# Performance work log

Hardware: AMD Instinct MI355X
Metric: run time of the kernel (lower is better)

Reference implementation:

```python
import jax, jax.numpy as jnp
import numpy as np

B, H, W, C = 8, 256, 256, 64
M1, M2 = 32, 32
SCALE = 1.0 / (C * C)


def setup_inputs() -> dict:
    key = jax.random.key(0)
    ku, k1, k2, k3, k4 = jax.random.split(key, 5)
    u = jax.random.normal(ku, (B, H, W, C), dtype=jnp.float32)
    wshape = (C, C, M1, M2)
    w_pos_r = SCALE * jax.random.normal(k1, wshape, dtype=jnp.float32)
    w_pos_i = SCALE * jax.random.normal(k2, wshape, dtype=jnp.float32)
    w_neg_r = SCALE * jax.random.normal(k3, wshape, dtype=jnp.float32)
    w_neg_i = SCALE * jax.random.normal(k4, wshape, dtype=jnp.float32)
    return {"u": u, "w_pos_r": w_pos_r, "w_pos_i": w_pos_i,
            "w_neg_r": w_neg_r, "w_neg_i": w_neg_i}


def _compl_mul2d(inp, weights):
    # inp: [B, m1, m2, Cin] complex; weights: [Cin, Cout, m1, m2] complex
    return jnp.einsum('bxyi,ioxy->bxyo', inp, weights)


def reference(u, w_pos_r, w_pos_i, w_neg_r, w_neg_i):
    b, h, w, c = u.shape
    wf = w // 2 + 1  # rfft size along W
    u_ft = jnp.fft.rfft2(u, axes=(1, 2))  # [B, H, Wf, C] complex
    w_pos = jax.lax.complex(w_pos_r, w_pos_i)
    w_neg = jax.lax.complex(w_neg_r, w_neg_i)
    top = _compl_mul2d(u_ft[:, :M1, :M2, :], w_pos)   # low positive freqs
    bot = _compl_mul2d(u_ft[:, h - M1:, :M2, :], w_neg)  # low negative freqs
    # out_ft zero-initialized, only truncated modes populated.
    # (Original allocates [B,H,W,C] but irfft2 with s=(H,W) only reads
    #  the first W//2+1 columns, which equals this [B,H,Wf,C] tensor.)
    out_ft = jnp.zeros((b, h, wf, c), dtype=u_ft.dtype)
    out_ft = out_ft.at[:, :M1, :M2, :].set(top)
    out_ft = out_ft.at[:, h - M1:, :M2, :].set(bot)
    # out_ft[:, -M1:M1] assignment in original is an empty slice (M1 <= H/2): no-op.
    return jnp.fft.irfft2(out_ft, s=(h, w), axes=(1, 2)).astype(u.dtype)
```

## Files before the change

kernel.cpp:

```cpp
#include <hip/hip_runtime.h>
#include <math.h>

#define BB 8
#define HH 256
#define WW 256
#define CC 64

__device__ inline void cmac(float2& a, float tx, float ty, float2 v) {
    a.x += tx * v.x - ty * v.y;
    a.y += tx * v.y + ty * v.x;
}
__device__ inline void fma4(float4& a, float s, float4 v) {
    a.x += s * v.x; a.y += s * v.y; a.z += s * v.z; a.w += s * v.w;
}

__global__ __launch_bounds__(256) void k_tw(float2* __restrict__ Tf,
                                            float2* __restrict__ Ti,
                                            float* __restrict__ Ty,
                                            float* __restrict__ T2) {
    int e = blockIdx.x * 256 + threadIdx.x;
    if (e < 16384) {
        int x = e >> 6;
        int j = e & 63;
        int kxa = j + ((j >> 5) * 192);
        int tt = (kxa * x) & 255;
        float ang = (float)tt * (6.283185307179586f / 256.0f);
        float s, c;
        sincosf(ang, &s, &c);
        Tf[(size_t)x * 64 + j] = make_float2(c, -s);
        const float k = 2.0f / 65536.0f;
        Ti[(size_t)j * 256 + x] = make_float2(c * k, s * k);
    } else {
        int f = e - 16384;
        if (f < 8192) {
            int yp = f >> 6;
            int col = f & 63;
            int par = (col >> 5) & 1;
            int cs = (col >> 4) & 1;
            int m = col & 15;
            int ky = 2 * m + par;
            int tt = (ky * yp) & 255;
            float ang = (float)tt * (6.283185307179586f / 256.0f);
            float s, c;
            sincosf(ang, &s, &c);
            Ty[f] = cs ? -s : c;
        } else {
            int g = f - 8192;
            int pi = g >> 12;
            int j = (g >> 7) & 31;
            int p = g & 127;
            int m = j >> 1, ri = j & 1;
            int ky = 2 * m + pi;
            int tt = (ky * p) & 255;
            float ang = (float)tt * (6.283185307179586f / 256.0f);
            float s, c;
            sincosf(ang, &s, &c);
            T2[g] = ri ? -s : c;
        }
    }
}

__global__ __launch_bounds__(128, 3) void k_fwd_y(const float* __restrict__ u,
                                                  const float* __restrict__ Ty,
                                                  float2* __restrict__ V) {
    __shared__ float ue[32 * 68];
    __shared__ float uo[32 * 68];
    __shared__ float Tt[32 * 68];

    int t = threadIdx.x;
    int b = blockIdx.x >> 8;
    int x = blockIdx.x & 255;
    int i8 = (t & 7) * 8;
    int w = t >> 3;
    int p = w & 1;
    int kyq = w >> 1;
    int yy = t >> 2;
    int c0 = (t & 3) * 16;

    const float* ub = u + ((size_t)(b * HH + x)) * (WW * CC);
    const float* uplane = p ? uo : ue;

    float4 A0r = {0,0,0,0}, A0i = {0,0,0,0};
    float4 B0r = {0,0,0,0}, B0i = {0,0,0,0};
    float4 A1r = {0,0,0,0}, A1i = {0,0,0,0};
    float4 B1r = {0,0,0,0}, B1i = {0,0,0,0};

    for (int yt = 0; yt < 4; ++yt) {
        const float* plo = ub + (size_t)(yt * 32 + yy) * CC + c0;
        const float* phi = plo + 128 * CC;
        float4 l0 = *(const float4*)(plo);
        float4 l1 = *(const float4*)(plo + 4);
        float4 l2 = *(const float4*)(plo + 8);
        float4 l3 = *(const float4*)(plo + 12);
        float4 h0 = *(const float4*)(phi);
        float4 h1 = *(const float4*)(phi + 4);
        float4 h2 = *(const float4*)(phi + 8);
        float4 h3 = *(const float4*)(phi + 12);
        const float* tsrc = Ty + (size_t)(yt * 32 + yy) * 64 + c0;
        float4 t0 = *(const float4*)(tsrc);
        float4 t1 = *(const float4*)(tsrc + 4);
        float4 t2 = *(const float4*)(tsrc + 8);
        float4 t3 = *(const float4*)(tsrc + 12);

        __syncthreads();
        int wb = yy * 68 + c0;
        *(float4*)(ue + wb)      = make_float4(l0.x+h0.x, l0.y+h0.y, l0.z+h0.z, l0.w+h0.w);
        *(float4*)(ue + wb + 4)  = make_float4(l1.x+h1.x, l1.y+h1.y, l1.z+h1.z, l1.w+h1.w);
        *(float4*)(ue + wb + 8)  = make_float4(l2.x+h2.x, l2.y+h2.y, l2.z+h2.z, l2.w+h2.w);
        *(float4*)(ue + wb + 12) = make_float4(l3.x+h3.x, l3.y+h3.y, l3.z+h3.z, l3.w+h3.w);
        *(float4*)(uo + wb)      = make_float4(l0.x-h0.x, l0.y-h0.y, l0.z-h0.z, l0.w-h0.w);
        *(float4*)(uo + wb + 4)  = make_float4(l1.x-h1.x, l1.y-h1.y, l1.z-h1.z, l1.w-h1.w);
        *(float4*)(uo + wb + 8)  = make_float4(l2.x-h2.x, l2.y-h2.y, l2.z-h2.z, l2.w-h2.w);
        *(float4*)(uo + wb + 12) = make_float4(l3.x-h3.x, l3.y-h3.y, l3.z-h3.z, l3.w-h3.w);
        *(float4*)(Tt + wb)      = t0;
        *(float4*)(Tt + wb + 4)  = t1;
        *(float4*)(Tt + wb + 8)  = t2;
        *(float4*)(Tt + wb + 12) = t3;
        __syncthreads();

        #pragma unroll
        for (int y2 = 0; y2 < 32; ++y2) {
            const float* tb = Tt + y2 * 68 + p * 32 + kyq * 2;
            float2 cp = *(const float2*)(tb);
            float2 sp = *(const float2*)(tb + 16);
            const float* up = uplane + y2 * 68 + i8;
            float4 uq0 = *(const float4*)(up);
            float4 uq1 = *(const float4*)(up + 4);
            fma4(A0r, cp.x, uq0);  fma4(A0i, sp.x, uq0);
            fma4(B0r, cp.x, uq1);  fma4(B0i, sp.x, uq1);
            fma4(A1r, cp.y, uq0);  fma4(A1i, sp.y, uq0);
            fma4(B1r, cp.y, uq1);  fma4(B1i, sp.y, uq1);
        }
    }

    {
        int ky = 4 * kyq + p;
        float2* vp = V + (size_t)(b * HH + x) * 2048 + ky * 64 + i8;
        *(float4*)(vp)     = make_float4(A0r.x, A0i.x, A0r.y, A0i.y);
        *(float4*)(vp + 2) = make_float4(A0r.z, A0i.z, A0r.w, A0i.w);
        *(float4*)(vp + 4) = make_float4(B0r.x, B0i.x, B0r.y, B0i.y);
        *(float4*)(vp + 6) = make_float4(B0r.z, B0i.z, B0r.w, B0i.w);
    }
    {
        int ky = 4 * kyq + 2 + p;
        float2* vp = V + (size_t)(b * HH + x) * 2048 + ky * 64 + i8;
        *(float4*)(vp)     = make_float4(A1r.x, A1i.x, A1r.y, A1i.y);
        *(float4*)(vp + 2) = make_float4(A1r.z, A1i.z, A1r.w, A1i.w);
        *(float4*)(vp + 4) = make_float4(B1r.x, B1i.x, B1r.y, B1i.y);
        *(float4*)(vp + 6) = make_float4(B1r.z, B1i.z, B1r.w, B1i.w);
    }
}

__global__ __launch_bounds__(256) void k_fwd_x(const float2* __restrict__ Tf,
                                               const float2* __restrict__ V,
                                               float2* __restrict__ U) {
    __shared__ float sRe[2 * 2048];
    __shared__ float sIm[2 * 2048];
    __shared__ float2 Ts[32 * 16];

    int bx = blockIdx.x;
    int jq = bx >> 8;
    int ky = bx & 31;
    int b  = (bx >> 5) & 7;
    int t = threadIdx.x;
    int jr = t >> 5;
    int ir = t & 31;

    float2 a00 = {0,0}, a01 = {0,0}, a10 = {0,0}, a11 = {0,0};

    const float2* vb = V + (size_t)b * (HH * 2048) + ky * 64;
    int vrow = t >> 3;
    int vcol = (t & 7) * 8;
    int tjj = (t & 7) * 2;
    int parOff = (jr & 1) * 2048;

    for (int x0 = 0; x0 < 128; x0 += 32) {
        const float2* plo = vb + (size_t)(x0 + vrow) * 2048 + vcol;
        const float2* phi = plo + 128 * 2048;
        float4 l0 = *(const float4*)(plo);
        float4 l1 = *(const float4*)(plo + 2);
        float4 l2 = *(const float4*)(plo + 4);
        float4 l3 = *(const float4*)(plo + 6);
        float4 h0 = *(const float4*)(phi);
        float4 h1 = *(const float4*)(phi + 2);
        float4 h2 = *(const float4*)(phi + 4);
        float4 h3 = *(const float4*)(phi + 6);
        float4 tv = *(const float4*)(Tf + (size_t)(x0 + vrow) * 64 + jq * 16 + tjj);

        __syncthreads();
        *(float4*)&Ts[vrow * 16 + tjj] = tv;
        int wb = vrow * 64 + vcol;
        *(float4*)(sRe + wb)            = make_float4(l0.x+h0.x, l0.z+h0.z, l1.x+h1.x, l1.z+h1.z);
        *(float4*)(sRe + wb + 4)        = make_float4(l2.x+h2.x, l2.z+h2.z, l3.x+h3.x, l3.z+h3.z);
        *(float4*)(sIm + wb)            = make_float4(l0.y+h0.y, l0.w+h0.w, l1.y+h1.y, l1.w+h1.w);
        *(float4*)(sIm + wb + 4)        = make_float4(l2.y+h2.y, l2.w+h2.w, l3.y+h3.y, l3.w+h3.w);
        *(float4*)(sRe + 2048 + wb)     = make_float4(l0.x-h0.x, l0.z-h0.z, l1.x-h1.x, l1.z-h1.z);
        *(float4*)(sRe + 2048 + wb + 4) = make_float4(l2.x-h2.x, l2.z-h2.z, l3.x-h3.x, l3.z-h3.z);
        *(float4*)(sIm + 2048 + wb)     = make_float4(l0.y-h0.y, l0.w-h0.w, l1.y-h1.y, l1.w-h1.w);
        *(float4*)(sIm + 2048 + wb + 4) = make_float4(l2.y-h2.y, l2.w-h2.w, l3.y-h3.y, l3.w-h3.w);
        __syncthreads();

        #pragma unroll
        for (int xx = 0; xx < 32; ++xx) {
            float2 t0 = Ts[xx * 16 + jr];
            float2 t1 = Ts[xx * 16 + jr + 8];
            const float* re = sRe + parOff + xx * 64;
            const float* im = sIm + parOff + xx * 64;
            float vr0 = re[ir], vr1 = re[ir + 32];
            float vi0 = im[ir], vi1 = im[ir + 32];
            a00.x += t0.x*vr0 - t0.y*vi0;  a00.y += t0.x*vi0 + t0.y*vr0;
            a01.x += t0.x*vr1 - t0.y*vi1;  a01.y += t0.x*vi1 + t0.y*vr1;
            a10.x += t1.x*vr0 - t1.y*vi0;  a10.y += t1.x*vi0 + t1.y*vr0;
            a11.x += t1.x*vr1 - t1.y*vi1;  a11.y += t1.x*vi1 + t1.y*vr1;
        }
    }

    int j0 = jq * 16 + jr;
    float2* u0 = U + ((size_t)(j0 * 32 + ky) * 8 + b) * 64 + ir;
    u0[0]  = a00;
    u0[32] = a01;
    float2* u1 = U + ((size_t)((j0 + 8) * 32 + ky) * 8 + b) * 64 + ir;
    u1[0]  = a10;
    u1[32] = a11;
}

__global__ __launch_bounds__(256) void k_modew(const float* __restrict__ wpr,
                                               const float* __restrict__ wpi,
                                               const float* __restrict__ wnr,
                                               const float* __restrict__ wni,
                                               const float2* __restrict__ U,
                                               float2* __restrict__ OF) {
    __shared__ float2 uS[4 * 8 * 64];
    __shared__ float2 wS[4 * 8 * 32];

    int bx = blockIdx.x;
    int j   = bx & 63;
    int kyt = (bx >> 6) & 7;
    int oh  = bx >> 9;
    int ky0 = kyt * 4;
    int sel = j >> 5, kxl = j & 31;
    const float* sr = sel ? wnr : wpr;
    const float* si = sel ? wni : wpi;
    int tid = threadIdx.x;

    const float2* up = U + (size_t)(j * 32 + ky0) * 512;
    #pragma unroll
    for (int k = 0; k < 8; ++k) uS[tid + 256 * k] = up[tid + 256 * k];

    int o32 = tid & 31;
    int bh  = tid >> 5;
    int irS = tid >> 5;
    int ooS = tid & 31;

    float2 acc[4];
    #pragma unroll
    for (int k = 0; k < 4; ++k) acc[k] = make_float2(0.f, 0.f);

    for (int it = 0; it < 8; ++it) {
        __syncthreads();
        {
            int ig = it * 8 + irS;
            int og = oh * 32 + ooS;
            size_t base = (((size_t)(ig * 64 + og)) * 32 + kxl) * 32 + ky0;
            float4 r0 = *(const float4*)(sr + base);
            float4 q0 = *(const float4*)(si + base);
            float2* wrow = wS + irS * 32 + ooS;
            wrow[0 * 256] = make_float2(r0.x, q0.x);
            wrow[1 * 256] = make_float2(r0.y, q0.y);
            wrow[2 * 256] = make_float2(r0.z, q0.z);
            wrow[3 * 256] = make_float2(r0.w, q0.w);
        }
        __syncthreads();
        #pragma unroll
        for (int ir = 0; ir < 8; ++ir) {
            int ig = it * 8 + ir;
            #pragma unroll
            for (int ky = 0; ky < 4; ++ky) {
                float2 wv = wS[ky * 256 + ir * 32 + o32];
                float2 uv = uS[ky * 512 + bh * 64 + ig];
                acc[ky].x += uv.x * wv.x - uv.y * wv.y;
                acc[ky].y += uv.x * wv.y + uv.y * wv.x;
            }
        }
    }

    int og = oh * 32 + o32;
    #pragma unroll
    for (int ky = 0; ky < 4; ++ky) {
        OF[((size_t)(bh * 32 + ky0 + ky) * 64 + j) * 64 + og] = acc[ky];
    }
}

__global__ __launch_bounds__(256) void k_inv_x(const float2* __restrict__ Ti,
                                               const float2* __restrict__ OF,
                                               float2* __restrict__ A) {
    __shared__ float2 Ts[32 * 32];
    __shared__ float2 Os[32 * 64];

    int bx = blockIdx.x;
    int xt = bx >> 8;
    int ky = bx & 31;
    int b  = (bx >> 5) & 7;
    int t = threadIdx.x;
    int or_ = t & 15;
    int xr = t >> 4;

    float2 acc[2][2][4];
    #pragma unroll
    for (int pa = 0; pa < 2; ++pa)
        #pragma unroll
        for (int p = 0; p < 2; ++p)
            #pragma unroll
            for (int q = 0; q < 4; ++q) acc[pa][p][q] = make_float2(0.f, 0.f);

    const float2* ofb = OF + (size_t)(b * 32 + ky) * 4096;
    int sj = t >> 3;
    int sx = (t & 7) * 4;
    int so = (t & 7) * 8;

    for (int kh = 0; kh < 2; ++kh) {
        const float2* tsrc = Ti + (size_t)(kh * 32 + sj) * 256 + xt * 32 + sx;
        float4 t0 = *(const float4*)(tsrc);
        float4 t1 = *(const float4*)(tsrc + 2);
        const float2* osrc = ofb + (size_t)(kh * 32 + sj) * 64 + so;
        float4 o0 = *(const float4*)(osrc);
        float4 o1 = *(const float4*)(osrc + 2);
        float4 o2 = *(const float4*)(osrc + 4);
        float4 o3 = *(const float4*)(osrc + 6);

        __syncthreads();
        *(float4*)&Ts[sj * 32 + sx]     = t0;
        *(float4*)&Ts[sj * 32 + sx + 2] = t1;
        float2* od = &Os[sj * 64 + so];
        *(float4*)(od)     = o0;
        *(float4*)(od + 2) = o1;
        *(float4*)(od + 4) = o2;
        *(float4*)(od + 6) = o3;
        __syncthreads();

        #pragma unroll
        for (int jj = 0; jj < 32; ++jj) {
            float4 tp = *(const float4*)&Ts[jj * 32 + xr * 2];
            float2 q0 = Os[jj * 64 + or_];
            float2 q1 = Os[jj * 64 + or_ + 16];
            float2 q2 = Os[jj * 64 + or_ + 32];
            float2 q3 = Os[jj * 64 + or_ + 48];
            const int pa = jj & 1;
            cmac(acc[pa][0][0], tp.x, tp.y, q0);
            cmac(acc[pa][0][1], tp.x, tp.y, q1);
            cmac(acc[pa][0][2], tp.x, tp.y, q2);
            cmac(acc[pa][0][3], tp.x, tp.y, q3);
            cmac(acc[pa][1][0], tp.z, tp.w, q0);
            cmac(acc[pa][1][1], tp.z, tp.w, q1);
            cmac(acc[pa][1][2], tp.z, tp.w, q2);
            cmac(acc[pa][1][3], tp.z, tp.w, q3);
        }
    }

    float sc = (ky == 0) ? 0.5f : 1.0f;
    #pragma unroll
    for (int p = 0; p < 2; ++p) {
        int x = xt * 32 + xr * 2 + p;
        float2* alo = A + ((size_t)(b * 256 + x) * 32 + ky) * 64 + or_;
        float2* ahi = A + ((size_t)(b * 256 + x + 128) * 32 + ky) * 64 + or_;
        #pragma unroll
        for (int q = 0; q < 4; ++q) {
            float2 se = acc[0][p][q], so2 = acc[1][p][q];
            alo[16 * q] = make_float2((se.x + so2.x) * sc, (se.y + so2.y) * sc);
            ahi[16 * q] = make_float2((se.x - so2.x) * sc, (se.y - so2.y) * sc);
        }
    }
}

__global__ __launch_bounds__(512, 2) void k_inv_y(const float* __restrict__ T2g,
                                                  const float2* __restrict__ A,
                                                  float* __restrict__ out) {
    __shared__ float As[2 * 32 * 68];
    __shared__ float T2s[2 * 32 * 132];

    int t = threadIdx.x;
    int b = blockIdx.x >> 8;
    int x = blockIdx.x & 255;
    int o4 = (t & 15) * 4;
    int pr = t >> 4;

    float acc[2][4][4];
    #pragma unroll
    for (int pi = 0; pi < 2; ++pi)
        #pragma unroll
        for (int pp = 0; pp < 4; ++pp)
            #pragma unroll
            for (int k = 0; k < 4; ++k) acc[pi][pp][k] = 0.f;

    {
        int ky = t >> 4;
        int oc = (t & 15) * 4;
        const float2* ap = A + (size_t)(b * 256 + x) * 2048 + ky * 64 + oc;
        float4 g0 = *(const float4*)(ap);
        float4 g1 = *(const float4*)(ap + 2);
        int pi = ky & 1, m = ky >> 1;
        float* re = As + ((pi * 32) + 2 * m) * 68 + oc;
        float* im = As + ((pi * 32) + 2 * m + 1) * 68 + oc;
        *(float4*)(re) = make_float4(g0.x, g0.z, g1.x, g1.z);
        *(float4*)(im) = make_float4(g0.y, g0.w, g1.y, g1.w);
    }
    {
        int row = t >> 3;
        int c = (t & 7) * 16;
        const float* tg = T2g + (size_t)row * 128 + c;
        float4 q0 = *(const float4*)(tg);
        float4 q1 = *(const float4*)(tg + 4);
        float4 q2 = *(const float4*)(tg + 8);
        float4 q3 = *(const float4*)(tg + 12);
        float* td = T2s + row * 132 + c;
        *(float4*)(td)      = q0;
        *(float4*)(td + 4)  = q1;
        *(float4*)(td + 8)  = q2;
        *(float4*)(td + 12) = q3;
    }
    __syncthreads();

    #pragma unroll
    for (int pi = 0; pi < 2; ++pi) {
        #pragma unroll
        for (int jj = 0; jj < 32; ++jj) {
            float4 ta = *(const float4*)(T2s + (pi * 32 + jj) * 132 + pr * 4);
            float4 av = *(const float4*)(As + (pi * 32 + jj) * 68 + o4);
            acc[pi][0][0] += ta.x * av.x;  acc[pi][0][1] += ta.x * av.y;
            acc[pi][0][2] += ta.x * av.z;  acc[pi][0][3] += ta.x * av.w;
            acc[pi][1][0] += ta.y * av.x;  acc[pi][1][1] += ta.y * av.y;
            acc[pi][1][2] += ta.y * av.z;  acc[pi][1][3] += ta.y * av.w;
            acc[pi][2][0] += ta.z * av.x;  acc[pi][2][1] += ta.z * av.y;
            acc[pi][2][2] += ta.z * av.z;  acc[pi][2][3] += ta.z * av.w;
            acc[pi][3][0] += ta.w * av.x;  acc[pi][3][1] += ta.w * av.y;
            acc[pi][3][2] += ta.w * av.z;  acc[pi][3][3] += ta.w * av.w;
        }
    }

    float* op = out + (size_t)(b * 256 + x) * (256 * 64);
    #pragma unroll
    for (int pp = 0; pp < 4; ++pp) {
        int p = pr * 4 + pp;
        float4 lo = make_float4(acc[0][pp][0] + acc[1][pp][0],
                                acc[0][pp][1] + acc[1][pp][1],
                                acc[0][pp][2] + acc[1][pp][2],
                                acc[0][pp][3] + acc[1][pp][3]);
        float4 hi = make_float4(acc[0][pp][0] - acc[1][pp][0],
                                acc[0][pp][1] - acc[1][pp][1],
                                acc[0][pp][2] - acc[1][pp][2],
                                acc[0][pp][3] - acc[1][pp][3]);
        *(float4*)(op + (size_t)p * 64 + o4)         = lo;
        *(float4*)(op + (size_t)(p + 128) * 64 + o4) = hi;
    }
}

extern "C" void kernel_launch(void* const* d_in, const int* in_sizes, int n_in,
                              void* d_out, int out_size, void* d_ws, size_t ws_size,
                              hipStream_t stream) {
    const float* u   = (const float*)d_in[0];
    const float* wpr = (const float*)d_in[1];
    const float* wpi = (const float*)d_in[2];
    const float* wnr = (const float*)d_in[3];
    const float* wni = (const float*)d_in[4];
    float* out = (float*)d_out;

    char* ws = (char*)d_ws;
    float2* U  = (float2*)(ws);
    float2* OF = (float2*)(ws + 8388608);
    float2* V  = (float2*)(ws + 16777216);
    float2* A  = V;
    float2* Tf = (float2*)(ws + 50331648);
    float2* Ti = (float2*)(ws + 50331648 + 131072);
    float*  Ty = (float*)(ws + 50331648 + 262144);
    float*  T2 = (float*)(ws + 50331648 + 262144 + 32768);

    k_tw<<<128, 256, 0, stream>>>(Tf, Ti, Ty, T2);
    k_fwd_y<<<BB * HH, 128, 0, stream>>>(u, Ty, V);
    k_fwd_x<<<1024, 256, 0, stream>>>(Tf, V, U);
    k_modew<<<1024, 256, 0, stream>>>(wpr, wpi, wnr, wni, U, OF);
    k_inv_x<<<1024, 256, 0, stream>>>(Ti, OF, A);
    k_inv_y<<<BB * HH, 512, 0, stream>>>(T2, A, out);
}
```

Baseline: 224.1 us.

## Retile forward-y and inverse-y DFT kernels for more register reuse per thread

k_fwd_y now processes four x rows per 256-thread block. Each thread computes four frequency pairs instead of two, using 16-row y tiles, so every twiddle tile loaded into shared memory is reused across four rows. k_inv_y drops from 512 to 128 threads per block, and each thread computes an 8x8 output tile instead of 4x4, which cuts shared-memory loads per FMA. The cost is higher register pressure and fewer threads in flight for latency hiding, with a risk of lower occupancy.

```diff
diff --git a/kernel.cpp b/kernel.cpp
--- a/kernel.cpp
+++ b/kernel.cpp
@@ -60,33 +60,41 @@
     }
 }
 
-__global__ __launch_bounds__(128, 3) void k_fwd_y(const float* __restrict__ u,
-                                                  const float* __restrict__ Ty,
-                                                  float2* __restrict__ V) {
-    __shared__ float ue[32 * 68];
-    __shared__ float uo[32 * 68];
-    __shared__ float Tt[32 * 68];
+__global__ __launch_bounds__(256) void k_fwd_y(const float* __restrict__ u,
+                                               const float* __restrict__ Ty,
+                                               float2* __restrict__ V) {
+    __shared__ float ue[4][16 * 68];
+    __shared__ float uo[4][16 * 68];
+    __shared__ float Tt[16 * 68];
 
     int t = threadIdx.x;
-    int b = blockIdx.x >> 8;
-    int x = blockIdx.x & 255;
-    int i8 = (t & 7) * 8;
-    int w = t >> 3;
+    int bx = blockIdx.x;
+    int b = bx >> 6;
+    int x4 = (bx & 63) * 4;
+    int r = t >> 6;
+    int l = t & 63;
+    int x = x4 + r;
+    int i8 = (l & 7) * 8;
+    int w = l >> 3;
     int p = w & 1;
-    int kyq = w >> 1;
-    int yy = t >> 2;
-    int c0 = (t & 3) * 16;
+    int kq = w >> 1;
+    int yy = l >> 2;
+    int c0 = (l & 3) * 16;
+    int trow = t >> 4;
+    int tc = (t & 15) * 4;
 
     const float* ub = u + ((size_t)(b * HH + x)) * (WW * CC);
-    const float* uplane = p ? uo : ue;
-
-    float4 A0r = {0,0,0,0}, A0i = {0,0,0,0};
-    float4 B0r = {0,0,0,0}, B0i = {0,0,0,0};
-    float4 A1r = {0,0,0,0}, A1i = {0,0,0,0};
-    float4 B1r = {0,0,0,0}, B1i = {0,0,0,0};
-
-    for (int yt = 0; yt < 4; ++yt) {
-        const float* plo = ub + (size_t)(yt * 32 + yy) * CC + c0;
+    const float* uplane = p ? uo[r] : ue[r];
+
+    float4 aR[4], aI[4], bR[4], bI[4];
+    #pragma unroll
+    for (int m = 0; m < 4; ++m) {
+        aR[m] = make_float4(0,0,0,0); aI[m] = make_float4(0,0,0,0);
+        bR[m] = make_float4(0,0,0,0); bI[m] = make_float4(0,0,0,0);
+    }
+
+    for (int yt = 0; yt < 8; ++yt) {
+        const float* plo = ub + (size_t)(yt * 16 + yy) * CC + c0;
         const float* phi = plo + 128 * CC;
         float4 l0 = *(const float4*)(plo);
         float4 l1 = *(const float4*)(plo + 4);
@@ -96,58 +104,53 @@
         float4 h1 = *(const float4*)(phi + 4);
         float4 h2 = *(const float4*)(phi + 8);
         float4 h3 = *(const float4*)(phi + 12);
-        const float* tsrc = Ty + (size_t)(yt * 32 + yy) * 64 + c0;
-        float4 t0 = *(const float4*)(tsrc);
-        float4 t1 = *(const float4*)(tsrc + 4);
-        float4 t2 = *(const float4*)(tsrc + 8);
-        float4 t3 = *(const float4*)(tsrc + 12);
+        float4 tv = *(const float4*)(Ty + (size_t)(yt * 16 + trow) * 64 + tc);
 
         __syncthreads();
         int wb = yy * 68 + c0;
-        *(float4*)(ue + wb)      = make_float4(l0.x+h0.x, l0.y+h0.y, l0.z+h0.z, l0.w+h0.w);
-        *(float4*)(ue + wb + 4)  = make_float4(l1.x+h1.x, l1.y+h1.y, l1.z+h1.z, l1.w+h1.w);
-        *(float4*)(ue + wb + 8)  = make_float4(l2.x+h2.x, l2.y+h2.y, l2.z+h2.z, l2.w+h2.w);
-        *(float4*)(ue + wb + 12) = make_float4(l3.x+h3.x, l3.y+h3.y, l3.z+h3.z, l3.w+h3.w);
-        *(float4*)(uo + wb)      = make_float4(l0.x-h0.x, l0.y-h0.y, l0.z-h0.z, l0.w-h0.w);
-        *(float4*)(uo + wb + 4)  = make_float4(l1.x-h1.x, l1.y-h1.y, l1.z-h1.z, l1.w-h1.w);
-        *(float4*)(uo + wb + 8)  = make_float4(l2.x-h2.x, l2.y-h2.y, l2.z-h2.z, l2.w-h2.w);
-        *(float4*)(uo + wb + 12) = make_float4(l3.x-h3.x, l3.y-h3.y, l3.z-h3.z, l3.w-h3.w);
-        *(float4*)(Tt + wb)      = t0;
-        *(float4*)(Tt + wb + 4)  = t1;
-        *(float4*)(Tt + wb + 8)  = t2;
-        *(float4*)(Tt + wb + 12) = t3;
-        __syncthreads();
-
-        #pragma unroll
-        for (int y2 = 0; y2 < 32; ++y2) {
-            const float* tb = Tt + y2 * 68 + p * 32 + kyq * 2;
-            float2 cp = *(const float2*)(tb);
-            float2 sp = *(const float2*)(tb + 16);
+        float* uer = ue[r];
+        float* uor = uo[r];
+        *(float4*)(uer + wb)      = make_float4(l0.x+h0.x, l0.y+h0.y, l0.z+h0.z, l0.w+h0.w);
+        *(float4*)(uer + wb + 4)  = make_float4(l1.x+h1.x, l1.y+h1.y, l1.z+h1.z, l1.w+h1.w);
+        *(float4*)(uer + wb + 8)  = make_float4(l2.x+h2.x, l2.y+h2.y, l2.z+h2.z, l2.w+h2.w);
+        *(float4*)(uer + wb + 12) = make_float4(l3.x+h3.x, l3.y+h3.y, l3.z+h3.z, l3.w+h3.w);
+        *(float4*)(uor + wb)      = make_float4(l0.x-h0.x, l0.y-h0.y, l0.z-h0.z, l0.w-h0.w);
+        *(float4*)(uor + wb + 4)  = make_float4(l1.x-h1.x, l1.y-h1.y, l1.z-h1.z, l1.w-h1.w);
+        *(float4*)(uor + wb + 8)  = make_float4(l2.x-h2.x, l2.y-h2.y, l2.z-h2.z, l2.w-h2.w);
+        *(float4*)(uor + wb + 12) = make_float4(l3.x-h3.x, l3.y-h3.y, l3.z-h3.z, l3.w-h3.w);
+        *(float4*)(Tt + trow * 68 + tc) = tv;
+        __syncthreads();
+
+        #pragma unroll
+        for (int y2 = 0; y2 < 16; ++y2) {
+            const float* tb = Tt + y2 * 68 + p * 32 + kq * 2;
+            float2 c01 = *(const float2*)(tb);
+            float2 c89 = *(const float2*)(tb + 8);
+            float2 s01 = *(const float2*)(tb + 16);
+            float2 s89 = *(const float2*)(tb + 24);
             const float* up = uplane + y2 * 68 + i8;
-            float4 uq0 = *(const float4*)(up);
-            float4 uq1 = *(const float4*)(up + 4);
-            fma4(A0r, cp.x, uq0);  fma4(A0i, sp.x, uq0);
-            fma4(B0r, cp.x, uq1);  fma4(B0i, sp.x, uq1);
-            fma4(A1r, cp.y, uq0);  fma4(A1i, sp.y, uq0);
-            fma4(B1r, cp.y, uq1);  fma4(B1i, sp.y, uq1);
-        }
-    }
-
-    {
-        int ky = 4 * kyq + p;
+            float4 u0 = *(const float4*)(up);
+            float4 u1 = *(const float4*)(up + 4);
+            fma4(aR[0], c01.x, u0);  fma4(bR[0], c01.x, u1);
+            fma4(aI[0], s01.x, u0);  fma4(bI[0], s01.x, u1);
+            fma4(aR[1], c01.y, u0);  fma4(bR[1], c01.y, u1);
+            fma4(aI[1], s01.y, u0);  fma4(bI[1], s01.y, u1);
+            fma4(aR[2], c89.x, u0);  fma4(bR[2], c89.x, u1);
+            fma4(aI[2], s89.x, u0);  fma4(bI[2], s89.x, u1);
+            fma4(aR[3], c89.y, u0);  fma4(bR[3], c89.y, u1);
+            fma4(aI[3], s89.y, u0);  fma4(bI[3], s89.y, u1);
+        }
+    }
+
+    int mv[4] = {2 * kq, 2 * kq + 1, 2 * kq + 8, 2 * kq + 9};
+    #pragma unroll
+    for (int mi = 0; mi < 4; ++mi) {
+        int ky = 2 * mv[mi] + p;
         float2* vp = V + (size_t)(b * HH + x) * 2048 + ky * 64 + i8;
-        *(float4*)(vp)     = make_float4(A0r.x, A0i.x, A0r.y, A0i.y);
-        *(float4*)(vp + 2) = make_float4(A0r.z, A0i.z, A0r.w, A0i.w);
-        *(float4*)(vp + 4) = make_float4(B0r.x, B0i.x, B0r.y, B0i.y);
-        *(float4*)(vp + 6) = make_float4(B0r.z, B0i.z, B0r.w, B0i.w);
-    }
-    {
-        int ky = 4 * kyq + 2 + p;
-        float2* vp = V + (size_t)(b * HH + x) * 2048 + ky * 64 + i8;
-        *(float4*)(vp)     = make_float4(A1r.x, A1i.x, A1r.y, A1i.y);
-        *(float4*)(vp + 2) = make_float4(A1r.z, A1i.z, A1r.w, A1i.w);
-        *(float4*)(vp + 4) = make_float4(B1r.x, B1i.x, B1r.y, B1i.y);
-        *(float4*)(vp + 6) = make_float4(B1r.z, B1i.z, B1r.w, B1i.w);
+        *(float4*)(vp)     = make_float4(aR[mi].x, aI[mi].x, aR[mi].y, aI[mi].y);
+        *(float4*)(vp + 2) = make_float4(aR[mi].z, aI[mi].z, aR[mi].w, aI[mi].w);
+        *(float4*)(vp + 4) = make_float4(bR[mi].x, bI[mi].x, bR[mi].y, bI[mi].y);
+        *(float4*)(vp + 6) = make_float4(bR[mi].z, bI[mi].z, bR[mi].w, bI[mi].w);
     }
 }
 
@@ -372,85 +375,102 @@
     }
 }
 
-__global__ __launch_bounds__(512, 2) void k_inv_y(const float* __restrict__ T2g,
-                                                  const float2* __restrict__ A,
-                                                  float* __restrict__ out) {
-    __shared__ float As[2 * 32 * 68];
-    __shared__ float T2s[2 * 32 * 132];
+__global__ __launch_bounds__(128) void k_inv_y(const float* __restrict__ T2g,
+                                               const float2* __restrict__ A,
+                                               float* __restrict__ out) {
+    __shared__ float As[64 * 68];
+    __shared__ float T2s[64 * 132];
 
     int t = threadIdx.x;
     int b = blockIdx.x >> 8;
     int x = blockIdx.x & 255;
-    int o4 = (t & 15) * 4;
-    int pr = t >> 4;
-
-    float acc[2][4][4];
-    #pragma unroll
-    for (int pi = 0; pi < 2; ++pi)
-        #pragma unroll
-        for (int pp = 0; pp < 4; ++pp)
-            #pragma unroll
-            for (int k = 0; k < 4; ++k) acc[pi][pp][k] = 0.f;
 
     {
-        int ky = t >> 4;
-        int oc = (t & 15) * 4;
+        int ky = t >> 2;
+        int oc = (t & 3) * 16;
         const float2* ap = A + (size_t)(b * 256 + x) * 2048 + ky * 64 + oc;
         float4 g0 = *(const float4*)(ap);
         float4 g1 = *(const float4*)(ap + 2);
+        float4 g2 = *(const float4*)(ap + 4);
+        float4 g3 = *(const float4*)(ap + 6);
+        float4 g4 = *(const float4*)(ap + 8);
+        float4 g5 = *(const float4*)(ap + 10);
+        float4 g6 = *(const float4*)(ap + 12);
+        float4 g7 = *(const float4*)(ap + 14);
         int pi = ky & 1, m = ky >> 1;
         float* re = As + ((pi * 32) + 2 * m) * 68 + oc;
         float* im = As + ((pi * 32) + 2 * m + 1) * 68 + oc;
-        *(float4*)(re) = make_float4(g0.x, g0.z, g1.x, g1.z);
-        *(float4*)(im) = make_float4(g0.y, g0.w, g1.y, g1.w);
+        *(float4*)(re)      = make_float4(g0.x, g0.z, g1.x, g1.z);
+        *(float4*)(re + 4)  = make_float4(g2.x, g2.z, g3.x, g3.z);
+        *(float4*)(re + 8)  = make_float4(g4.x, g4.z, g5.x, g5.z);
+        *(float4*)(re + 12) = make_float4(g6.x, g6.z, g7.x, g7.z);
+        *(float4*)(im)      = make_float4(g0.y, g0.w, g1.y, g1.w);
+        *(float4*)(im + 4)  = make_float4(g2.y, g2.w, g3.y, g3.w);
+        *(float4*)(im + 8)  = make_float4(g4.y, g4.w, g5.y, g5.w);
+        *(float4*)(im + 12) = make_float4(g6.y, g6.w, g7.y, g7.w);
     }
     {
-        int row = t >> 3;
-        int c = (t & 7) * 16;
+        int row = t >> 1;
+        int c = (t & 1) * 64;
         const float* tg = T2g + (size_t)row * 128 + c;
-        float4 q0 = *(const float4*)(tg);
-        float4 q1 = *(const float4*)(tg + 4);
-        float4 q2 = *(const float4*)(tg + 8);
-        float4 q3 = *(const float4*)(tg + 12);
         float* td = T2s + row * 132 + c;
-        *(float4*)(td)      = q0;
-        *(float4*)(td + 4)  = q1;
-        *(float4*)(td + 8)  = q2;
-        *(float4*)(td + 12) = q3;
+        #pragma unroll
+        for (int k = 0; k < 16; ++k) {
+            float4 q = *(const float4*)(tg + 4 * k);
+            *(float4*)(td + 4 * k) = q;
+        }
     }
     __syncthreads();
 
+    int pr = t >> 3;
+    int o8 = (t & 7) * 8;
+
+    float4 acc[2][8][2];
+    #pragma unroll
+    for (int pi = 0; pi < 2; ++pi)
+        #pragma unroll
+        for (int pp = 0; pp < 8; ++pp) {
+            acc[pi][pp][0] = make_float4(0,0,0,0);
+            acc[pi][pp][1] = make_float4(0,0,0,0);
+        }
+
     #pragma unroll
     for (int pi = 0; pi < 2; ++pi) {
         #pragma unroll
         for (int jj = 0; jj < 32; ++jj) {
-            float4 ta = *(const float4*)(T2s + (pi * 32 + jj) * 132 + pr * 4);
-            float4 av = *(const float4*)(As + (pi * 32 + jj) * 68 + o4);
-            acc[pi][0][0] += ta.x * av.x;  acc[pi][0][1] += ta.x * av.y;
-            acc[pi][0][2] += ta.x * av.z;  acc[pi][0][3] += ta.x * av.w;
-            acc[pi][1][0] += ta.y * av.x;  acc[pi][1][1] += ta.y * av.y;
-            acc[pi][1][2] += ta.y * av.z;  acc[pi][1][3] += ta.y * av.w;
-            acc[pi][2][0] += ta.z * av.x;  acc[pi][2][1] += ta.z * av.y;
-            acc[pi][2][2] += ta.z * av.z;  acc[pi][2][3] += ta.z * av.w;
-            acc[pi][3][0] += ta.w * av.x;  acc[pi][3][1] += ta.w * av.y;
-            acc[pi][3][2] += ta.w * av.z;  acc[pi][3][3] += ta.w * av.w;
+            const float* trow = T2s + (pi * 32 + jj) * 132 + pr * 8;
+            float4 ta = *(const float4*)(trow);
+            float4 tb = *(const float4*)(trow + 4);
+            const float* arow = As + (pi * 32 + jj) * 68 + o8;
+            float4 av0 = *(const float4*)(arow);
+            float4 av1 = *(const float4*)(arow + 4);
+            float tp0 = ta.x, tp1 = ta.y, tp2 = ta.z, tp3 = ta.w;
+            float tp4 = tb.x, tp5 = tb.y, tp6 = tb.z, tp7 = tb.w;
+            fma4(acc[pi][0][0], tp0, av0);  fma4(acc[pi][0][1], tp0, av1);
+            fma4(acc[pi][1][0], tp1, av0);  fma4(acc[pi][1][1], tp1, av1);
+            fma4(acc[pi][2][0], tp2, av0);  fma4(acc[pi][2][1], tp2, av1);
+            fma4(acc[pi][3][0], tp3, av0);  fma4(acc[pi][3][1], tp3, av1);
+            fma4(acc[pi][4][0], tp4, av0);  fma4(acc[pi][4][1], tp4, av1);
+            fma4(acc[pi][5][0], tp5, av0);  fma4(acc[pi][5][1], tp5, av1);
+            fma4(acc[pi][6][0], tp6, av0);  fma4(acc[pi][6][1], tp6, av1);
+            fma4(acc[pi][7][0], tp7, av0);  fma4(acc[pi][7][1], tp7, av1);
         }
     }
 
     float* op = out + (size_t)(b * 256 + x) * (256 * 64);
     #pragma unroll
-    for (int pp = 0; pp < 4; ++pp) {
-        int p = pr * 4 + pp;
-        float4 lo = make_float4(acc[0][pp][0] + acc[1][pp][0],
-                                acc[0][pp][1] + acc[1][pp][1],
-                                acc[0][pp][2] + acc[1][pp][2],
-                                acc[0][pp][3] + acc[1][pp][3]);
-        float4 hi = make_float4(acc[0][pp][0] - acc[1][pp][0],
-                                acc[0][pp][1] - acc[1][pp][1],
-                                acc[0][pp][2] - acc[1][pp][2],
-                                acc[0][pp][3] - acc[1][pp][3]);
-        *(float4*)(op + (size_t)p * 64 + o4)         = lo;
-        *(float4*)(op + (size_t)(p + 128) * 64 + o4) = hi;
+    for (int pp = 0; pp < 8; ++pp) {
+        int p = pr * 8 + pp;
+        float4 e0 = acc[0][pp][0], e1 = acc[0][pp][1];
+        float4 d0 = acc[1][pp][0], d1 = acc[1][pp][1];
+        *(float4*)(op + (size_t)p * 64 + o8)
+            = make_float4(e0.x+d0.x, e0.y+d0.y, e0.z+d0.z, e0.w+d0.w);
+        *(float4*)(op + (size_t)p * 64 + o8 + 4)
+            = make_float4(e1.x+d1.x, e1.y+d1.y, e1.z+d1.z, e1.w+d1.w);
+        *(float4*)(op + (size_t)(p + 128) * 64 + o8)
+            = make_float4(e0.x-d0.x, e0.y-d0.y, e0.z-d0.z, e0.w-d0.w);
+        *(float4*)(op + (size_t)(p + 128) * 64 + o8 + 4)
+            = make_float4(e1.x-d1.x, e1.y-d1.y, e1.z-d1.z, e1.w-d1.w);
     }
 }
 
@@ -475,9 +495,9 @@
     float*  T2 = (float*)(ws + 50331648 + 262144 + 32768);
 
     k_tw<<<128, 256, 0, stream>>>(Tf, Ti, Ty, T2);
-    k_fwd_y<<<BB * HH, 128, 0, stream>>>(u, Ty, V);
+    k_fwd_y<<<512, 256, 0, stream>>>(u, Ty, V);
     k_fwd_x<<<1024, 256, 0, stream>>>(Tf, V, U);
     k_modew<<<1024, 256, 0, stream>>>(wpr, wpi, wnr, wni, U, OF);
     k_inv_x<<<1024, 256, 0, stream>>>(Ti, OF, A);
-    k_inv_y<<<BB * HH, 512, 0, stream>>>(T2, A, out);
-}
+    k_inv_y<<<BB * HH, 128, 0, stream>>>(T2, A, out);
+}
```

Measured after the change: 252.4 us. 12.7% more time.
